# Kernel optimization log

Hardware: AMD Instinct MI355X
Metric: run time of the kernel (lower is better)

Reference implementation:

```python
import jax, jax.numpy as jnp
import numpy as np

N, E, B = 65536, 524288, 256
FEAT, EMB, NH, NB, NC = 64, 128, 4, 2, 4
OUT = EMB // NH
SLOPE = 0.01  # LeakyReLU negative_slope used everywhere in the module


def lrelu(x):
    return jnp.where(x > 0, x, SLOPE * x)


def seg_softmax(logits, seg, nseg, mask):
    # PyG softmax(src, batch): exp(x - segment_max) / (segment_sum + 1e-16)
    z = jnp.where(mask, logits, -jnp.inf)
    m = jax.ops.segment_max(z, seg, num_segments=nseg)
    m = jnp.where(jnp.isfinite(m), m, 0.0)
    e = jnp.exp(z - m[seg])
    s = jax.ops.segment_sum(e, seg, num_segments=nseg)
    return e / (s[seg] + 1e-16)


def topk_pool(x, seg, w, min_score, nseg):
    # PyG TopKPooling with min_score: score = softmax(x.w, batch);
    # keep nodes with score > min(min_score, per-graph max - 1e-7); x_out = x*score.
    score = x @ w  # [N]
    sm = seg_softmax(score, seg, nseg, jnp.ones(score.shape, bool))
    smax = jax.ops.segment_max(sm, seg, num_segments=nseg)
    thr = jnp.minimum(smax - 1e-7, min_score)
    keep = sm > thr[seg]
    xp = jnp.where(keep[:, None], x * sm[:, None], 0.0)
    return xp, keep


def graph_conv_max(x, src, dst, emask, Wrel, Wroot, b, n):
    # PyG GraphConv(aggr='max'): out = Wrel @ max_{j in N(i)} x_j + Wroot @ x_i + b
    msg = jnp.where(emask[:, None], x[src], -jnp.inf)  # [E, d]
    agg = jax.ops.segment_max(msg, dst, num_segments=n)
    agg = jnp.where(jnp.isfinite(agg), agg, 0.0)  # nodes with no in-edges -> 0 (PyG scatter fill)
    return agg @ Wrel.T + x @ Wroot.T + b


def batchnorm(x, g, b):
    # training-mode BatchNorm1d: batch statistics, biased variance, eps=1e-5
    mu = x.mean(0)
    var = x.var(0)
    return g * (x - mu) * jax.lax.rsqrt(var + 1e-5) + b


def setup_inputs() -> dict:
    key = jax.random.key(0)
    ks = jax.random.split(key, 16)
    s_feat = np.float32(1.0 / np.sqrt(FEAT))
    s_emb = np.float32(1.0 / np.sqrt(EMB))
    return {
        "x": jax.random.normal(ks[0], (N, FEAT), jnp.float32),
        "edge_index": jax.random.randint(ks[1], (2, E), 0, N, jnp.int32),
        "batch": (jnp.arange(N, dtype=jnp.int32) // (N // B)).astype(jnp.int32),
        "W_rel0": jax.random.normal(ks[2], (EMB, FEAT), jnp.float32) * s_feat,
        "W_root0": jax.random.normal(ks[3], (EMB, FEAT), jnp.float32) * s_feat,
        "b0": jnp.zeros((EMB,), jnp.float32),
        "bn0_g": jnp.ones((EMB,), jnp.float32),
        "bn0_b": jnp.zeros((EMB,), jnp.float32),
        "blk_pool_w": jax.random.normal(ks[4], (NB, NH, EMB), jnp.float32) * s_emb,
        "blk_Wrel": jax.random.normal(ks[5], (NB, NH, OUT, EMB), jnp.float32) * s_emb,
        "blk_Wroot": jax.random.normal(ks[6], (NB, NH, OUT, EMB), jnp.float32) * s_emb,
        "blk_b": jnp.zeros((NB, NH, OUT), jnp.float32),
        "blk_bn_g": jnp.ones((NB, EMB), jnp.float32),
        "blk_bn_b": jnp.zeros((NB, EMB), jnp.float32),
        "cls_pool_w": jax.random.normal(ks[7], (NC, EMB), jnp.float32) * s_emb,
        "cls_gW1": jax.random.normal(ks[8], (NC, EMB, EMB), jnp.float32) * s_emb,
        "cls_gb1": jnp.zeros((NC, EMB), jnp.float32),
        "cls_gW2": jax.random.normal(ks[9], (NC, EMB), jnp.float32) * s_emb,
        "cls_gb2": jnp.zeros((NC,), jnp.float32),
        "cls_fW1": jax.random.normal(ks[10], (NC, EMB, EMB), jnp.float32) * s_emb,
        "cls_fb1": jnp.zeros((NC, EMB), jnp.float32),
        "cls_fW2": jax.random.normal(ks[11], (NC, EMB), jnp.float32) * s_emb,
        "cls_fb2": jnp.zeros((NC,), jnp.float32),
        "batch_size": B,
    }


def reference(x, edge_index, batch, W_rel0, W_root0, b0, bn0_g, bn0_b,
              blk_pool_w, blk_Wrel, blk_Wroot, blk_b, blk_bn_g, blk_bn_b,
              cls_pool_w, cls_gW1, cls_gb1, cls_gW2, cls_gb2,
              cls_fW1, cls_fb1, cls_fW2, cls_fb2, batch_size):
    n = x.shape[0]
    src, dst = edge_index[0], edge_index[1]
    all_e = jnp.ones(src.shape, bool)
    # conv0 -> leaky_relu -> bn0
    h = lrelu(graph_conv_max(x, src, dst, all_e, W_rel0, W_root0, b0, n))
    cur = batchnorm(h, bn0_g, bn0_b)
    # multi-head blocks: pool (min_score=0.7) -> GraphConv(max) per head, scatter
    # back to original node slots, concat heads, bn, residual 0.5*(x + 0.5*bn(new))
    for bi in range(NB):
        heads = []
        for hi in range(NH):
            xp, keep = topk_pool(cur, batch, blk_pool_w[bi, hi], 0.7, batch_size)
            emask = keep[src] & keep[dst]
            o = lrelu(graph_conv_max(xp, src, dst, emask,
                                     blk_Wrel[bi, hi], blk_Wroot[bi, hi],
                                     blk_b[bi, hi], n))
            heads.append(jnp.where(keep[:, None], o, 0.0))
        new = batchnorm(jnp.concatenate(heads, axis=-1), blk_bn_g[bi], blk_bn_b[bi])
        cur = 0.5 * (cur + 0.5 * new)
    # classification heads: pool (min_score=0.8) -> GlobalAttention -> MLP -> 1
    outs = []
    for c in range(NC):
        xp, keep = topk_pool(cur, batch, cls_pool_w[c], 0.8, batch_size)
        gate = lrelu(xp @ cls_gW1[c].T + cls_gb1[c]) @ cls_gW2[c] + cls_gb2[c]  # [N]
        a = seg_softmax(gate, batch, batch_size, keep)
        pooled = jax.ops.segment_sum(a[:, None] * xp, batch, num_segments=batch_size)  # [B, EMB]
        y = lrelu(pooled @ cls_fW1[c].T + cls_fb1[c]) @ cls_fW2[c] + cls_fb2[c]  # [B]
        outs.append(y)
    logits = jnp.stack(outs, axis=-1)  # [B, NC]
    return jax.nn.log_softmax(logits, axis=-1)
```

## Files before the change

kernel.cpp:

```cpp
#include <hip/hip_runtime.h>
#include <math.h>

#define NN 65536
#define NE 524288
#define NG 256
#define SLOPE 0.01f
#define CAP 131072

__device__ __forceinline__ float lrelu(float v){ return v > 0.f ? v : SLOPE*v; }

__device__ __forceinline__ float blockMax4(float v, float* s4){
  #pragma unroll
  for(int o=32;o>0;o>>=1) v = fmaxf(v, __shfl_down(v, o, 64));
  int t = threadIdx.x;
  __syncthreads();
  if((t&63)==0) s4[t>>6] = v;
  __syncthreads();
  return fmaxf(fmaxf(s4[0], s4[1]), fmaxf(s4[2], s4[3]));
}
__device__ __forceinline__ float blockSum4(float v, float* s4){
  #pragma unroll
  for(int o=32;o>0;o>>=1) v += __shfl_down(v, o, 64);
  int t = threadIdx.x;
  __syncthreads();
  if((t&63)==0) s4[t>>6] = v;
  __syncthreads();
  return (s4[0]+s4[1])+(s4[2]+s4[3]);
}

__global__ __launch_bounds__(256) void k_count(const int* __restrict__ ei, int* __restrict__ deg){
  int e = blockIdx.x*256 + threadIdx.x;
  if(e < NE) atomicAdd(&deg[ei[NE + e]], 1);
}

__global__ __launch_bounds__(1024) void k_scan(const int* __restrict__ deg,
      int* __restrict__ offs, int* __restrict__ cursor){
  __shared__ int part[1024];
  int t = threadIdx.x;
  const int4* d4 = (const int4*)(deg + t*64);
  int4 buf[16];
  int s=0;
  #pragma unroll
  for(int i=0;i<16;i++){ buf[i]=d4[i]; s += buf[i].x+buf[i].y+buf[i].z+buf[i].w; }
  part[t]=s;
  __syncthreads();
  for(int off=1; off<1024; off<<=1){
    int v = (t>=off)? part[t-off] : 0;
    __syncthreads();
    part[t] += v;
    __syncthreads();
  }
  int run = (t==0)? 0 : part[t-1];
  #pragma unroll
  for(int i=0;i<16;i++){
    int4 d = buf[i];
    int4 o;
    o.x = run; run += d.x;
    o.y = run; run += d.y;
    o.z = run; run += d.z;
    o.w = run; run += d.w;
    ((int4*)(offs + t*64))[i] = o;
    ((int4*)(cursor + t*64))[i] = o;
  }
  if(t==1023) offs[NN] = run;
}

__global__ __launch_bounds__(256) void k_scatter(const int* __restrict__ ei,
      int* __restrict__ cursor, int* __restrict__ csr){
  int e = blockIdx.x*256 + threadIdx.x;
  if(e < NE){
    int d = ei[NE + e];
    int p = atomicAdd(&cursor[d], 1);
    csr[p] = ei[e];
  }
}

__global__ __launch_bounds__(256) void k_agg0(const float* __restrict__ x,
    const int* __restrict__ offs, const int* __restrict__ csr, float* __restrict__ agg0){
  int tid = blockIdx.x*256 + threadIdx.x;
  int node = tid>>4, q = tid&15;
  int e0 = offs[node], e1 = offs[node+1];
  float4 acc = make_float4(0.f,0.f,0.f,0.f);
  if(e0 < e1){
    acc = make_float4(-INFINITY,-INFINITY,-INFINITY,-INFINITY);
    int e = e0;
    for(; e+7 < e1; e += 8){
      int si[8];
      #pragma unroll
      for(int u=0;u<8;u++) si[u] = csr[e+u];
      float4 v[8];
      #pragma unroll
      for(int u=0;u<8;u++) v[u] = ((const float4*)x)[si[u]*16 + q];
      #pragma unroll
      for(int u=0;u<8;u++){
        acc.x=fmaxf(acc.x,v[u].x); acc.y=fmaxf(acc.y,v[u].y);
        acc.z=fmaxf(acc.z,v[u].z); acc.w=fmaxf(acc.w,v[u].w);
      }
    }
    for(; e < e1; e++){
      int s0 = csr[e];
      float4 v0 = ((const float4*)x)[s0*16 + q];
      acc.x=fmaxf(acc.x,v0.x); acc.y=fmaxf(acc.y,v0.y);
      acc.z=fmaxf(acc.z,v0.z); acc.w=fmaxf(acc.w,v0.w);
    }
  }
  ((float4*)agg0)[node*16 + q] = acc;
}

__global__ __launch_bounds__(256, 2) void k_conv0mm(
    const float* __restrict__ agg0, const float* __restrict__ x,
    const float* __restrict__ Wrel, const float* __restrict__ Wroot,
    const float* __restrict__ b0, float* __restrict__ cur,
    float* __restrict__ bnsum, float* __restrict__ bnsq){
  __shared__ float4 As[2048];
  const int t = threadIdx.x;
  const int tn = t & 15;
  const int tc = t >> 4;
  float acc[8][8];
  #pragma unroll
  for(int i=0;i<8;i++)
    #pragma unroll
    for(int j=0;j<8;j++) acc[i][j]=0.f;

  const size_t tileoff = (size_t)blockIdx.x * 8192;
  #pragma unroll 1
  for(int ch=0; ch<2; ch++){
    const float4* gA = (const float4*)((ch==0? agg0 : x) + tileoff);
    const float4* gW = (const float4*)(ch==0? Wrel : Wroot);
    __syncthreads();
    #pragma unroll
    for(int i=0;i<8;i++){
      int idx = t + i*256;
      int n = idx>>4, k4 = idx&15;
      As[n*16 + ((k4 + (n>>3))&15)] = gA[idx];
    }
    __syncthreads();
    #pragma unroll 1
    for(int k4=0;k4<16;k4++){
      float4 a4[8];
      #pragma unroll
      for(int i=0;i<8;i++) a4[i] = As[(tn*8+i)*16 + ((k4+tn)&15)];
      #pragma unroll
      for(int j=0;j<8;j++){
        float4 w4 = gW[(tc*8+j)*16 + k4];
        #pragma unroll
        for(int i=0;i<8;i++){
          acc[i][j] = fmaf(a4[i].x, w4.x, acc[i][j]);
          acc[i][j] = fmaf(a4[i].y, w4.y, acc[i][j]);
          acc[i][j] = fmaf(a4[i].z, w4.z, acc[i][j]);
          acc[i][j] = fmaf(a4[i].w, w4.w, acc[i][j]);
        }
      }
    }
  }

  float bj[8];
  #pragma unroll
  for(int j=0;j<8;j++) bj[j] = b0[tc*8+j];
  float cs[8], cq[8];
  #pragma unroll
  for(int j=0;j<8;j++){ cs[j]=0.f; cq[j]=0.f; }
  const int nbase = blockIdx.x*128;
  #pragma unroll
  for(int i=0;i<8;i++){
    int node = nbase + tn*8 + i;
    float v[8];
    #pragma unroll
    for(int j=0;j<8;j++){
      v[j] = lrelu(acc[i][j] + bj[j]);
      cs[j] += v[j]; cq[j] += v[j]*v[j];
    }
    float4 o0 = make_float4(v[0],v[1],v[2],v[3]);
    float4 o1 = make_float4(v[4],v[5],v[6],v[7]);
    ((float4*)cur)[node*32 + tc*2 + 0] = o0;
    ((float4*)cur)[node*32 + tc*2 + 1] = o1;
  }
  __syncthreads();
  float* reds = (float*)As;
  float* redq = ((float*)As) + 2048;
  #pragma unroll
  for(int j=0;j<8;j++){
    reds[(tc*8+j)*16 + tn] = cs[j];
    redq[(tc*8+j)*16 + tn] = cq[j];
  }
  __syncthreads();
  if(t<128){
    float S=0.f, Q=0.f;
    #pragma unroll
    for(int i=0;i<16;i++){ S += reds[t*16+i]; Q += redq[t*16+i]; }
    atomicAdd(&bnsum[t], S);
    atomicAdd(&bnsq[t], Q);
  }
}

__global__ __launch_bounds__(256) void k_scores(const float* __restrict__ cur0,
    const float* __restrict__ bns0, const float* __restrict__ bnq0,
    const float* __restrict__ g0,
    const float* __restrict__ pw0, const float* __restrict__ pw1,
    const float* __restrict__ pwc,
    float* __restrict__ scores0, float* __restrict__ pre1, float* __restrict__ pre2){
  __shared__ __align__(16) float w[12][128];
  __shared__ float sc0s[128];
  const int t = threadIdx.x;
  if(t<128){
    float mu = bns0[t]*(1.0f/NN);
    float var = bnq0[t]*(1.0f/NN) - mu*mu;
    sc0s[t] = g0[t]*rsqrtf(var+1e-5f);
  }
  __syncthreads();
  for(int i=t;i<512;i+=256){
    int h=i>>7, j=i&127;
    float s = sc0s[j];
    w[h][j]   = pw0[i]*s;
    w[4+h][j] = pw1[i]*(0.5f*s);
    w[8+h][j] = pwc[i]*(0.25f*s);
  }
  __syncthreads();
  const int tid = blockIdx.x*256 + t;
  const int n = tid>>5, k = tid&31;
  float4 v = ((const float4*)cur0)[tid];
  float a[12];
  #pragma unroll
  for(int q=0;q<12;q++){
    float4 wv = *(const float4*)&w[q][k*4];
    a[q] = v.x*wv.x + v.y*wv.y + v.z*wv.z + v.w*wv.w;
  }
  #pragma unroll
  for(int o=16;o>0;o>>=1){
    #pragma unroll
    for(int q=0;q<12;q++) a[q] += __shfl_down(a[q], o, 32);
  }
  if(k==0){
    ((float4*)scores0)[n] = make_float4(a[0],a[1],a[2],a[3]);
    ((float4*)pre1)[n]    = make_float4(a[4],a[5],a[6],a[7]);
    ((float4*)pre2)[n]    = make_float4(a[8],a[9],a[10],a[11]);
  }
}

__global__ __launch_bounds__(256) void k_poolselW(const float* __restrict__ scores,
    float minscore, float* __restrict__ sm4, int* __restrict__ cnt,
    int* __restrict__ wl, int* __restrict__ idxP){
  const int t = threadIdx.x, g = blockIdx.x;
  const int h = t>>6, l = t&63;
  const int n0 = g*256;
  float s[4];
  #pragma unroll
  for(int i=0;i<4;i++) s[i] = scores[(size_t)(n0 + l + i*64)*4 + h];
  float m = fmaxf(fmaxf(s[0],s[1]),fmaxf(s[2],s[3]));
  #pragma unroll
  for(int o=32;o>0;o>>=1) m = fmaxf(m, __shfl_xor(m, o, 64));
  float e[4], es=0.f;
  #pragma unroll
  for(int i=0;i<4;i++){ e[i]=expf(s[i]-m); es+=e[i]; }
  #pragma unroll
  for(int o=32;o>0;o>>=1) es += __shfl_xor(es, o, 64);
  float inv = 1.f/(es+1e-16f);
  float sm[4];
  float mx = -INFINITY;
  #pragma unroll
  for(int i=0;i<4;i++){ sm[i]=e[i]*inv; mx=fmaxf(mx,sm[i]); }
  #pragma unroll
  for(int o=32;o>0;o>>=1) mx = fmaxf(mx, __shfl_xor(mx, o, 64));
  float thr = fminf(mx - 1e-7f, minscore);
  #pragma unroll
  for(int i=0;i<4;i++){
    int n = n0 + l + i*64;
    sm4[(size_t)n*4 + h] = sm[i];
    int slot = -1;
    if(sm[i] > thr){
      int p = atomicAdd(cnt, 1);
      if(p < CAP){ slot = p; wl[p] = (h<<16) | n; }
    }
    idxP[(size_t)h*NN + n] = slot;
  }
}

__global__ __launch_bounds__(256) void k_blockconv0(const float* __restrict__ cur0,
    const int* __restrict__ offs, const int* __restrict__ csr,
    const int* __restrict__ idxP, const float* __restrict__ sm4,
    const int* __restrict__ cnt, const int* __restrict__ wl,
    const float* __restrict__ Wrel, const float* __restrict__ Wroot,
    const float* __restrict__ bias,
    float* __restrict__ new1c, float* __restrict__ bnsum, float* __restrict__ bnsq,
    const float* __restrict__ bns0, const float* __restrict__ bnq0,
    const float* __restrict__ g0, const float* __restrict__ b0bn){
  __shared__ __align__(16) float aggs[8][128];
  __shared__ __align__(16) float xps[8][128];
  __shared__ __align__(16) float scv[128];
  __shared__ __align__(16) float ofv[128];
  const int t = threadIdx.x, grp = t>>5, lane = t&31;
  if(t<128){
    float mu = bns0[t]*(1.0f/NN);
    float var = bnq0[t]*(1.0f/NN) - mu*mu;
    float sv = g0[t]*rsqrtf(var+1e-5f);
    scv[t]=sv; ofv[t]=b0bn[t]-mu*sv;
  }
  __syncthreads();
  const float4 s4l = *(const float4*)&scv[lane*4];
  const float4 o4l = *(const float4*)&ofv[lane*4];
  int total = *cnt; if(total > CAP) total = CAP;
  for(int item = blockIdx.x*8 + grp; item < total; item += gridDim.x*8){
    const int wv = wl[item];
    const int h = wv>>16, n = wv & 0xFFFF;
    const size_t hn = (size_t)h*NN;
    const float smn = sm4[(size_t)n*4+h];
    const int e0 = offs[n], e1 = offs[n+1];
    float4 acc = make_float4(-INFINITY,-INFINITY,-INFINITY,-INFINITY);
    bool any = false;
    for(int e=e0;e<e1;e++){
      int s = csr[e];
      if(idxP[hn + s] >= 0){
        any = true;
        float sv = sm4[(size_t)s*4+h];
        float4 v = ((const float4*)cur0)[s*32 + lane];
        v.x = (v.x*s4l.x + o4l.x)*sv; v.y = (v.y*s4l.y + o4l.y)*sv;
        v.z = (v.z*s4l.z + o4l.z)*sv; v.w = (v.w*s4l.w + o4l.w)*sv;
        acc.x = fmaxf(acc.x, v.x); acc.y = fmaxf(acc.y, v.y);
        acc.z = fmaxf(acc.z, v.z); acc.w = fmaxf(acc.w, v.w);
      }
    }
    if(!any) acc = make_float4(0.f,0.f,0.f,0.f);
    *(float4*)&aggs[grp][lane*4] = acc;
    float4 xv = ((const float4*)cur0)[n*32 + lane];
    xv.x = (xv.x*s4l.x + o4l.x)*smn; xv.y = (xv.y*s4l.y + o4l.y)*smn;
    xv.z = (xv.z*s4l.z + o4l.z)*smn; xv.w = (xv.w*s4l.w + o4l.w)*smn;
    *(float4*)&xps[grp][lane*4] = xv;
    const float* Wr = Wrel  + (size_t)(h*32+lane)*128;
    const float* Wo = Wroot + (size_t)(h*32+lane)*128;
    float o = bias[h*32+lane];
    for(int k=0;k<32;k++){
      float4 a  = *(const float4*)&aggs[grp][k*4];
      float4 xx = *(const float4*)&xps[grp][k*4];
      float4 wr = ((const float4*)Wr)[k];
      float4 wo = ((const float4*)Wo)[k];
      o += a.x*wr.x + a.y*wr.y + a.z*wr.z + a.w*wr.w;
      o += xx.x*wo.x + xx.y*wo.y + xx.z*wo.z + xx.w*wo.w;
    }
    o = lrelu(o);
    new1c[(size_t)item*32 + lane] = o;
    atomicAdd(&bnsum[h*32+lane], o);
    atomicAdd(&bnsq[h*32+lane], o*o);
  }
}

__global__ __launch_bounds__(256) void k_poolsel1(
    const float* __restrict__ pre1, float* __restrict__ pre2,
    const int* __restrict__ cnt0, const int* __restrict__ wl0,
    const float* __restrict__ new1c,
    const float* __restrict__ bnsA, const float* __restrict__ bnqA,
    const float* __restrict__ g1v,
    const float* __restrict__ pw1, const float* __restrict__ pwc,
    float minscore, float* __restrict__ sm4out,
    int* __restrict__ cnt1, int* __restrict__ wl1, int* __restrict__ idx1P){
  __shared__ float s1s[128];
  __shared__ __align__(16) float w1s[4][128];
  __shared__ __align__(16) float wcs[4][128];
  __shared__ float patch1[256][4];
  const int t = threadIdx.x, g = blockIdx.x;
  if(t<128){
    float mu = bnsA[t]*(1.0f/NN);
    float var = bnqA[t]*(1.0f/NN) - mu*mu;
    s1s[t] = g1v[t]*rsqrtf(var+1e-5f);
  }
  for(int i=t;i<512;i+=256){ w1s[i>>7][i&127]=pw1[i]; wcs[i>>7][i&127]=pwc[i]; }
  #pragma unroll
  for(int h=0;h<4;h++) patch1[t][h]=0.f;
  __syncthreads();
  int total0 = *cnt0; if(total0 > CAP) total0 = CAP;
  for(int i=t; i<total0; i+=256){
    int wv = wl0[i];
    int n = wv & 0xFFFF, hp = wv>>16;
    if((n>>8)==g){
      int nl = n & 255;
      float d[4]={0.f,0.f,0.f,0.f}, d2[4]={0.f,0.f,0.f,0.f};
      for(int l=0;l<32;l++){
        int j = hp*32+l;
        float base = new1c[(size_t)i*32+l] * s1s[j];
        #pragma unroll
        for(int h=0;h<4;h++){ d[h]+=base*w1s[h][j]; d2[h]+=base*wcs[h][j]; }
      }
      #pragma unroll
      for(int h=0;h<4;h++){
        atomicAdd(&patch1[nl][h], 0.25f*d[h]);
        atomicAdd(&pre2[n*4+h], 0.125f*d2[h]);
      }
    }
  }
  __syncthreads();
  const int h = t>>6, l = t&63;
  const int n0 = g*256;
  float s[4];
  #pragma unroll
  for(int i=0;i<4;i++){
    int nl = l + i*64;
    s[i] = pre1[(size_t)(n0+nl)*4 + h] + patch1[nl][h];
  }
  float m = fmaxf(fmaxf(s[0],s[1]),fmaxf(s[2],s[3]));
  #pragma unroll
  for(int o=32;o>0;o>>=1) m = fmaxf(m, __shfl_xor(m, o, 64));
  float e[4], es=0.f;
  #pragma unroll
  for(int i=0;i<4;i++){ e[i]=expf(s[i]-m); es+=e[i]; }
  #pragma unroll
  for(int o=32;o>0;o>>=1) es += __shfl_xor(es, o, 64);
  float inv = 1.f/(es+1e-16f);
  float sm[4];
  float mx = -INFINITY;
  #pragma unroll
  for(int i=0;i<4;i++){ sm[i]=e[i]*inv; mx=fmaxf(mx,sm[i]); }
  #pragma unroll
  for(int o=32;o>0;o>>=1) mx = fmaxf(mx, __shfl_xor(mx, o, 64));
  float thr = fminf(mx - 1e-7f, minscore);
  #pragma unroll
  for(int i=0;i<4;i++){
    int n = n0 + l + i*64;
    sm4out[(size_t)n*4 + h] = sm[i];
    int slot = -1;
    if(sm[i] > thr){
      int p = atomicAdd(cnt1, 1);
      if(p < CAP){ slot = p; wl1[p] = (h<<16) | n; }
    }
    idx1P[(size_t)h*NN + n] = slot;
  }
}

__global__ __launch_bounds__(256) void k_blockconv1(const float* __restrict__ cur0,
    const int* __restrict__ offs, const int* __restrict__ csr,
    const int* __restrict__ idx0P, const float* __restrict__ new1c,
    const int* __restrict__ idx1P, const float* __restrict__ sm41,
    const int* __restrict__ cnt1, const int* __restrict__ wl1,
    const float* __restrict__ Wrel, const float* __restrict__ Wroot,
    const float* __restrict__ bias,
    float* __restrict__ new2c, float* __restrict__ bnsum, float* __restrict__ bnsq,
    const float* __restrict__ bns0, const float* __restrict__ bnq0,
    const float* __restrict__ g0, const float* __restrict__ b0bn,
    const float* __restrict__ bnsA, const float* __restrict__ bnqA,
    const float* __restrict__ g1v, const float* __restrict__ b1v){
  __shared__ __align__(16) float aggs[8][128];
  __shared__ __align__(16) float xps[8][128];
  __shared__ __align__(16) float sc0s[128], of0s[128], s1s[128], o1s[128];
  const int t = threadIdx.x, grp = t>>5, lane = t&31;
  if(t<128){
    float mu = bns0[t]*(1.0f/NN);
    float var = bnq0[t]*(1.0f/NN) - mu*mu;
    float sv = g0[t]*rsqrtf(var+1e-5f);
    sc0s[t]=sv; of0s[t]=b0bn[t]-mu*sv;
    float mu1 = bnsA[t]*(1.0f/NN);
    float var1 = bnqA[t]*(1.0f/NN) - mu1*mu1;
    float s1 = g1v[t]*rsqrtf(var1+1e-5f);
    s1s[t]=s1; o1s[t]=b1v[t]-mu1*s1;
  }
  __syncthreads();
  const float4 s0l = *(const float4*)&sc0s[lane*4];
  const float4 o0l = *(const float4*)&of0s[lane*4];
  const float4 s1l = *(const float4*)&s1s[lane*4];
  const float4 o1l = *(const float4*)&o1s[lane*4];
  const int hb = lane>>3;
  const size_t hbn = (size_t)hb*NN;
  int total = *cnt1; if(total > CAP) total = CAP;
  for(int item = blockIdx.x*8 + grp; item < total; item += gridDim.x*8){
    const int wv = wl1[item];
    const int h = wv>>16, n = wv & 0xFFFF;
    const size_t hn = (size_t)h*NN;
    const float smn = sm41[(size_t)n*4+h];
    const int e0 = offs[n], e1 = offs[n+1];
    float4 acc = make_float4(-INFINITY,-INFINITY,-INFINITY,-INFINITY);
    bool any = false;
    for(int e=e0;e<e1;e++){
      int s = csr[e];
      if(idx1P[hn + s] >= 0){
        any = true;
        float sv = sm41[(size_t)s*4+h];
        float4 c0 = ((const float4*)cur0)[s*32 + lane];
        float4 v;
        v.x = 0.5f*(s0l.x*c0.x+o0l.x) + 0.25f*o1l.x;
        v.y = 0.5f*(s0l.y*c0.y+o0l.y) + 0.25f*o1l.y;
        v.z = 0.5f*(s0l.z*c0.z+o0l.z) + 0.25f*o1l.z;
        v.w = 0.5f*(s0l.w*c0.w+o0l.w) + 0.25f*o1l.w;
        int i0 = idx0P[hbn + s];
        if(i0 >= 0){
          float4 nv = ((const float4*)(new1c + (size_t)i0*32))[lane&7];
          v.x += 0.25f*s1l.x*nv.x; v.y += 0.25f*s1l.y*nv.y;
          v.z += 0.25f*s1l.z*nv.z; v.w += 0.25f*s1l.w*nv.w;
        }
        v.x*=sv; v.y*=sv; v.z*=sv; v.w*=sv;
        acc.x = fmaxf(acc.x, v.x); acc.y = fmaxf(acc.y, v.y);
        acc.z = fmaxf(acc.z, v.z); acc.w = fmaxf(acc.w, v.w);
      }
    }
    if(!any) acc = make_float4(0.f,0.f,0.f,0.f);
    *(float4*)&aggs[grp][lane*4] = acc;
    {
      float4 c0 = ((const float4*)cur0)[n*32 + lane];
      float4 v;
      v.x = 0.5f*(s0l.x*c0.x+o0l.x) + 0.25f*o1l.x;
      v.y = 0.5f*(s0l.y*c0.y+o0l.y) + 0.25f*o1l.y;
      v.z = 0.5f*(s0l.z*c0.z+o0l.z) + 0.25f*o1l.z;
      v.w = 0.5f*(s0l.w*c0.w+o0l.w) + 0.25f*o1l.w;
      int i0 = idx0P[hbn + n];
      if(i0 >= 0){
        float4 nv = ((const float4*)(new1c + (size_t)i0*32))[lane&7];
        v.x += 0.25f*s1l.x*nv.x; v.y += 0.25f*s1l.y*nv.y;
        v.z += 0.25f*s1l.z*nv.z; v.w += 0.25f*s1l.w*nv.w;
      }
      v.x*=smn; v.y*=smn; v.z*=smn; v.w*=smn;
      *(float4*)&xps[grp][lane*4] = v;
    }
    const float* Wr = Wrel  + (size_t)(h*32+lane)*128;
    const float* Wo = Wroot + (size_t)(h*32+lane)*128;
    float o = bias[h*32+lane];
    for(int k=0;k<32;k++){
      float4 a  = *(const float4*)&aggs[grp][k*4];
      float4 xx = *(const float4*)&xps[grp][k*4];
      float4 wr = ((const float4*)Wr)[k];
      float4 wo = ((const float4*)Wo)[k];
      o += a.x*wr.x + a.y*wr.y + a.z*wr.z + a.w*wr.w;
      o += xx.x*wo.x + xx.y*wo.y + xx.z*wo.z + xx.w*wo.w;
    }
    o = lrelu(o);
    new2c[(size_t)item*32 + lane] = o;
    atomicAdd(&bnsum[h*32+lane], o);
    atomicAdd(&bnsq[h*32+lane], o*o);
  }
}

__global__ __launch_bounds__(256) void k_cls2(const float* __restrict__ cur0,
    const int* __restrict__ idx0P, const float* __restrict__ new1c,
    const int* __restrict__ idx1P, const float* __restrict__ new2c,
    const float* __restrict__ pre2, const int* __restrict__ cnt1,
    const int* __restrict__ wl1, const float* __restrict__ pwc,
    const float* __restrict__ bns0, const float* __restrict__ bnq0,
    const float* __restrict__ g0, const float* __restrict__ b0bn,
    const float* __restrict__ bnsA, const float* __restrict__ bnqA,
    const float* __restrict__ g1v, const float* __restrict__ b1v,
    const float* __restrict__ bnsB, const float* __restrict__ bnqB,
    const float* __restrict__ g2v, const float* __restrict__ b2v,
    const float* __restrict__ gW1, const float* __restrict__ gb1,
    const float* __restrict__ gW2, const float* __restrict__ gb2,
    const float* __restrict__ fW1, const float* __restrict__ fb1,
    const float* __restrict__ fW2, const float* __restrict__ fb2,
    float* __restrict__ yws){
  __shared__ float red[4];
  __shared__ float sc0s[128], of0s[128], s1s[128], o1s[128], s2s[128], o2s[128];
  __shared__ float wc[128];
  __shared__ float patch[256];
  __shared__ int keptL[256];
  __shared__ float keptS[256];
  __shared__ float gateL[256];
  __shared__ __align__(16) float xk[128];
  __shared__ __align__(16) float pooled[128];
  __shared__ int nkept;
  const int t = threadIdx.x;
  const int g = blockIdx.x >> 2, c = blockIdx.x & 3;
  if(t<128){
    float mu = bns0[t]*(1.0f/NN);
    float var = bnq0[t]*(1.0f/NN) - mu*mu;
    float sv = g0[t]*rsqrtf(var+1e-5f);
    sc0s[t]=sv; of0s[t]=b0bn[t]-mu*sv;
    float mu1 = bnsA[t]*(1.0f/NN);
    float var1 = bnqA[t]*(1.0f/NN) - mu1*mu1;
    float s1 = g1v[t]*rsqrtf(var1+1e-5f);
    s1s[t]=s1; o1s[t]=b1v[t]-mu1*s1;
    float mu2 = bnsB[t]*(1.0f/NN);
    float var2 = bnqB[t]*(1.0f/NN) - mu2*mu2;
    float s2 = g2v[t]*rsqrtf(var2+1e-5f);
    s2s[t]=s2; o2s[t]=b2v[t]-mu2*s2;
    wc[t] = pwc[c*128+t];
  }
  patch[t]=0.f;
  __syncthreads();
  int total1 = *cnt1; if(total1 > CAP) total1 = CAP;
  for(int i=t; i<total1; i+=256){
    int wv = wl1[i];
    int n = wv & 0xFFFF, hp = wv>>16;
    if((n>>8)==g){
      float d=0.f;
      for(int l=0;l<32;l++){
        int j = hp*32+l;
        d += new2c[(size_t)i*32+l]*s2s[j]*wc[j];
      }
      atomicAdd(&patch[n&255], 0.25f*d);
    }
  }
  __syncthreads();
  const int n = g*256 + t;
  float sc = pre2[n*4 + c] + patch[t];
  float m = blockMax4(sc, red);
  float e = expf(sc-m);
  float ssum = blockSum4(e, red);
  float sm = e/(ssum+1e-16f);
  float smax = blockMax4(sm, red);
  float thr = fminf(smax - 1e-7f, 0.8f);
  if(t==0) nkept = 0;
  __syncthreads();
  if(sm > thr){
    int p = atomicAdd(&nkept,1);
    keptL[p]=t; keptS[p]=sm;
  }
  __syncthreads();
  const int K = nkept;
  for(int k=0;k<K;k++){
    int ln = keptL[k]; float sv = keptS[k];
    int nn = g*256 + ln;
    if(t<32){
      float4 c0 = ((const float4*)cur0)[nn*32 + t];
      float4 s0l = *(const float4*)&sc0s[t*4];
      float4 o0l = *(const float4*)&of0s[t*4];
      float4 s1l = *(const float4*)&s1s[t*4];
      float4 o1l = *(const float4*)&o1s[t*4];
      float4 s2l = *(const float4*)&s2s[t*4];
      float4 o2l = *(const float4*)&o2s[t*4];
      int hb = t>>3;
      float4 v1;
      v1.x = 0.5f*(s0l.x*c0.x+o0l.x) + 0.25f*o1l.x;
      v1.y = 0.5f*(s0l.y*c0.y+o0l.y) + 0.25f*o1l.y;
      v1.z = 0.5f*(s0l.z*c0.z+o0l.z) + 0.25f*o1l.z;
      v1.w = 0.5f*(s0l.w*c0.w+o0l.w) + 0.25f*o1l.w;
      int i0 = idx0P[(size_t)hb*NN + nn];
      if(i0 >= 0){
        float4 nv = ((const float4*)(new1c + (size_t)i0*32))[t&7];
        v1.x += 0.25f*s1l.x*nv.x; v1.y += 0.25f*s1l.y*nv.y;
        v1.z += 0.25f*s1l.z*nv.z; v1.w += 0.25f*s1l.w*nv.w;
      }
      float4 v2;
      v2.x = 0.5f*v1.x + 0.25f*o2l.x;
      v2.y = 0.5f*v1.y + 0.25f*o2l.y;
      v2.z = 0.5f*v1.z + 0.25f*o2l.z;
      v2.w = 0.5f*v1.w + 0.25f*o2l.w;
      int i1 = idx1P[(size_t)hb*NN + nn];
      if(i1 >= 0){
        float4 nv = ((const float4*)(new2c + (size_t)i1*32))[t&7];
        v2.x += 0.25f*s2l.x*nv.x; v2.y += 0.25f*s2l.y*nv.y;
        v2.z += 0.25f*s2l.z*nv.z; v2.w += 0.25f*s2l.w*nv.w;
      }
      v2.x*=sv; v2.y*=sv; v2.z*=sv; v2.w*=sv;
      *(float4*)&xk[t*4] = v2;
    }
    __syncthreads();
    float part = 0.f;
    if(t<128){
      const float* W = gW1 + (size_t)c*16384 + (size_t)t*128;
      float a = gb1[c*128+t];
      for(int f=0;f<32;f++){
        float4 xv = *(const float4*)&xk[f*4];
        float4 wv = ((const float4*)W)[f];
        a += xv.x*wv.x + xv.y*wv.y + xv.z*wv.z + xv.w*wv.w;
      }
      part = lrelu(a) * gW2[c*128+t];
    }
    float gs = blockSum4(part, red);
    if(t==0) gateL[k] = gs + gb2[c];
    __syncthreads();
  }
  float gv = (t<K)? gateL[t] : -INFINITY;
  float gm = blockMax4(gv, red);
  float ge = (t<K)? expf(gv-gm) : 0.f;
  float gsum = blockSum4(ge, red);
  if(t<K) gateL[t] = ge/(gsum+1e-16f);
  __syncthreads();
  if(t<128){
    int hb = t>>5, l = t&31;
    float acc = 0.f;
    for(int k=0;k<K;k++){
      int nn = g*256 + keptL[k];
      float c0 = cur0[(size_t)nn*128 + t];
      float v1 = 0.5f*(sc0s[t]*c0 + of0s[t]) + 0.25f*o1s[t];
      int i0 = idx0P[(size_t)hb*NN + nn];
      if(i0 >= 0) v1 += 0.25f*s1s[t]*new1c[(size_t)i0*32 + l];
      float v2 = 0.5f*v1 + 0.25f*o2s[t];
      int i1 = idx1P[(size_t)hb*NN + nn];
      if(i1 >= 0) v2 += 0.25f*s2s[t]*new2c[(size_t)i1*32 + l];
      acc += gateL[k]*keptS[k]*v2;
    }
    pooled[t]=acc;
  }
  __syncthreads();
  float part2=0.f;
  if(t<128){
    const float* F = fW1 + (size_t)c*16384 + (size_t)t*128;
    float a = fb1[c*128+t];
    for(int f=0;f<32;f++){
      float4 xv = *(const float4*)&pooled[f*4];
      float4 wv = ((const float4*)F)[f];
      a += xv.x*wv.x + xv.y*wv.y + xv.z*wv.z + xv.w*wv.w;
    }
    part2 = lrelu(a) * fW2[c*128+t];
  }
  float ysum = blockSum4(part2, red);
  if(t==0) yws[g*4+c] = ysum + fb2[c];
}

__global__ __launch_bounds__(256) void k_clsfin(const float* __restrict__ yws,
                                                float* __restrict__ out){
  const int g = threadIdx.x;
  float4 y = ((const float4*)yws)[g];
  float m = fmaxf(fmaxf(y.x,y.y), fmaxf(y.z,y.w));
  float l = logf(expf(y.x-m)+expf(y.y-m)+expf(y.z-m)+expf(y.w-m));
  ((float4*)out)[g] = make_float4(y.x-m-l, y.y-m-l, y.z-m-l, y.w-m-l);
}

extern "C" void kernel_launch(void* const* d_in, const int* in_sizes, int n_in,
                              void* d_out, int out_size, void* d_ws, size_t ws_size,
                              hipStream_t stream){
  (void)in_sizes; (void)n_in; (void)out_size; (void)ws_size;
  const float* x     = (const float*)d_in[0];
  const int*   ei    = (const int*)d_in[1];
  const float* Wrel0 = (const float*)d_in[3];
  const float* Wroot0= (const float*)d_in[4];
  const float* b0    = (const float*)d_in[5];
  const float* bn0g  = (const float*)d_in[6];
  const float* bn0b  = (const float*)d_in[7];
  const float* bpw   = (const float*)d_in[8];
  const float* bWrel = (const float*)d_in[9];
  const float* bWroot= (const float*)d_in[10];
  const float* bbv   = (const float*)d_in[11];
  const float* bbng  = (const float*)d_in[12];
  const float* bbnb  = (const float*)d_in[13];
  const float* cpw   = (const float*)d_in[14];
  const float* gW1   = (const float*)d_in[15];
  const float* gb1   = (const float*)d_in[16];
  const float* gW2   = (const float*)d_in[17];
  const float* gb2   = (const float*)d_in[18];
  const float* fW1   = (const float*)d_in[19];
  const float* fb1   = (const float*)d_in[20];
  const float* fW2   = (const float*)d_in[21];
  const float* fb2   = (const float*)d_in[22];

  char* ws = (char*)d_ws;
  float* cur0  = (float*)(ws + 0);
  float* new1c = (float*)(ws + 33554432ull);
  float* new2c = (float*)(ws + 50331648ull);
  float* agg0  = new2c;
  int*   csr   = (int*)(ws + 67108864ull);
  float* scores0=(float*)(ws + 69206016ull);
  float* sm40  = scores0;
  float* pre1  = (float*)(ws + 70254592ull);
  float* sm41  = pre1;
  float* pre2  = (float*)(ws + 71303168ull);
  int*   wl0   = (int*)(ws + 72351744ull);
  int*   wl1   = (int*)(ws + 72876032ull);
  int*   offs  = (int*)(ws + 73400320ull);
  int*   cursor= (int*)(ws + 73666560ull);
  int*   idx0P = (int*)(ws + 73928704ull);
  int*   idx1P = (int*)(ws + 74977280ull);
  char*  Z     = ws + 76025856ull;
  int*   deg   = (int*)Z;
  float* bnsum0= (float*)(Z + 262144);
  float* bnsq0 = (float*)(Z + 262656);
  float* bnA   = (float*)(Z + 263168);
  float* bqA   = (float*)(Z + 263680);
  float* bnB   = (float*)(Z + 264192);
  float* bqB   = (float*)(Z + 264704);
  int*   cnt0  = (int*)(Z + 265216);
  int*   cnt1  = (int*)(Z + 265220);
  float* yws   = (float*)(Z + 266240);

  hipMemsetAsync(Z, 0, 270336, stream);

  k_count  <<<2048,256,0,stream>>>(ei, deg);
  k_scan   <<<1,1024,0,stream>>>(deg, offs, cursor);
  k_scatter<<<2048,256,0,stream>>>(ei, cursor, csr);

  k_agg0    <<<4096,256,0,stream>>>(x, offs, csr, agg0);
  k_conv0mm <<<512,256,0,stream>>>(agg0, x, Wrel0, Wroot0, b0, cur0, bnsum0, bnsq0);

  k_scores<<<8192,256,0,stream>>>(cur0, bnsum0, bnsq0, bn0g,
                                  bpw, bpw + 512, cpw, scores0, pre1, pre2);

  k_poolselW<<<256,256,0,stream>>>(scores0, 0.7f, sm40, cnt0, wl0, idx0P);

  k_blockconv0<<<256,256,0,stream>>>(cur0, offs, csr, idx0P, sm40, cnt0, wl0,
                                     bWrel, bWroot, bbv, new1c, bnA, bqA,
                                     bnsum0, bnsq0, bn0g, bn0b);

  k_poolsel1<<<256,256,0,stream>>>(pre1, pre2, cnt0, wl0, new1c,
                                   bnA, bqA, bbng,
                                   bpw + 512, cpw,
                                   0.7f, sm41, cnt1, wl1, idx1P);

  k_blockconv1<<<256,256,0,stream>>>(cur0, offs, csr, idx0P, new1c,
                                     idx1P, sm41, cnt1, wl1,
                                     bWrel + 16384, bWroot + 16384, bbv + 128,
                                     new2c, bnB, bqB,
                                     bnsum0, bnsq0, bn0g, bn0b,
                                     bnA, bqA, bbng, bbnb);

  k_cls2<<<1024,256,0,stream>>>(cur0, idx0P, new1c, idx1P, new2c,
                                pre2, cnt1, wl1, cpw,
                                bnsum0, bnsq0, bn0g, bn0b,
                                bnA, bqA, bbng, bbnb,
                                bnB, bqB, bbng + 128, bbnb + 128,
                                gW1, gb1, gW2, gb2, fW1, fb1, fW2, fb2, yws);
  k_clsfin<<<1,256,0,stream>>>(yws, (float*)d_out);
}
```

Baseline: 379.5 us.

## Stage conv0 weights in LDS, pad agg0 gather tail, fuse final log-softmax

The layer-0 GEMM now stages the weight tile in shared memory with the same swizzle as the activations and partially unrolls the k loop, instead of reading weights from global memory in the inner loop. The CSR max-gather drops its scalar tail loop and clamps indices to the last edge, so every iteration does a full 8-wide batch. Repeated reads are harmless for a max. The final log-softmax kernel is removed: the last of the four class blocks per graph, detected with an atomic counter, computes it, which saves one launch. This doubles shared memory in the GEMM, which may reduce occupancy, and the tail now does some redundant loads.

```diff
diff --git a/kernel.cpp b/kernel.cpp
--- a/kernel.cpp
+++ b/kernel.cpp
@@ -83,11 +83,14 @@
   float4 acc = make_float4(0.f,0.f,0.f,0.f);
   if(e0 < e1){
     acc = make_float4(-INFINITY,-INFINITY,-INFINITY,-INFINITY);
-    int e = e0;
-    for(; e+7 < e1; e += 8){
+    const int last = e1 - 1;
+    for(int e=e0; e<e1; e+=8){
       int si[8];
       #pragma unroll
-      for(int u=0;u<8;u++) si[u] = csr[e+u];
+      for(int u=0;u<8;u++){
+        int ee = e+u; ee = ee<last? ee : last;
+        si[u] = csr[ee];
+      }
       float4 v[8];
       #pragma unroll
       for(int u=0;u<8;u++) v[u] = ((const float4*)x)[si[u]*16 + q];
@@ -97,12 +100,6 @@
         acc.z=fmaxf(acc.z,v[u].z); acc.w=fmaxf(acc.w,v[u].w);
       }
     }
-    for(; e < e1; e++){
-      int s0 = csr[e];
-      float4 v0 = ((const float4*)x)[s0*16 + q];
-      acc.x=fmaxf(acc.x,v0.x); acc.y=fmaxf(acc.y,v0.y);
-      acc.z=fmaxf(acc.z,v0.z); acc.w=fmaxf(acc.w,v0.w);
-    }
   }
   ((float4*)agg0)[node*16 + q] = acc;
 }
@@ -113,6 +110,7 @@
     const float* __restrict__ b0, float* __restrict__ cur,
     float* __restrict__ bnsum, float* __restrict__ bnsq){
   __shared__ float4 As[2048];
+  __shared__ float4 Ws[2048];
   const int t = threadIdx.x;
   const int tn = t & 15;
   const int tc = t >> 4;
@@ -132,25 +130,27 @@
     for(int i=0;i<8;i++){
       int idx = t + i*256;
       int n = idx>>4, k4 = idx&15;
-      As[n*16 + ((k4 + (n>>3))&15)] = gA[idx];
+      int sw = n*16 + ((k4 + (n>>3))&15);
+      As[sw] = gA[idx];
+      Ws[sw] = gW[idx];
     }
     __syncthreads();
-    #pragma unroll 1
+    #pragma unroll 4
     for(int k4=0;k4<16;k4++){
-      float4 a4[8];
+      float4 a4[8], w4[8];
       #pragma unroll
       for(int i=0;i<8;i++) a4[i] = As[(tn*8+i)*16 + ((k4+tn)&15)];
       #pragma unroll
-      for(int j=0;j<8;j++){
-        float4 w4 = gW[(tc*8+j)*16 + k4];
+      for(int i=0;i<8;i++) w4[i] = Ws[(tc*8+i)*16 + ((k4+tc)&15)];
+      #pragma unroll
+      for(int i=0;i<8;i++)
         #pragma unroll
-        for(int i=0;i<8;i++){
-          acc[i][j] = fmaf(a4[i].x, w4.x, acc[i][j]);
-          acc[i][j] = fmaf(a4[i].y, w4.y, acc[i][j]);
-          acc[i][j] = fmaf(a4[i].z, w4.z, acc[i][j]);
-          acc[i][j] = fmaf(a4[i].w, w4.w, acc[i][j]);
+        for(int j=0;j<8;j++){
+          acc[i][j] = fmaf(a4[i].x, w4[j].x, acc[i][j]);
+          acc[i][j] = fmaf(a4[i].y, w4[j].y, acc[i][j]);
+          acc[i][j] = fmaf(a4[i].z, w4[j].z, acc[i][j]);
+          acc[i][j] = fmaf(a4[i].w, w4[j].w, acc[i][j]);
         }
-      }
     }
   }
 
@@ -177,7 +177,7 @@
   }
   __syncthreads();
   float* reds = (float*)As;
-  float* redq = ((float*)As) + 2048;
+  float* redq = (float*)Ws;
   #pragma unroll
   for(int j=0;j<8;j++){
     reds[(tc*8+j)*16 + tn] = cs[j];
@@ -539,7 +539,7 @@
     const float* __restrict__ gW2, const float* __restrict__ gb2,
     const float* __restrict__ fW1, const float* __restrict__ fb1,
     const float* __restrict__ fW2, const float* __restrict__ fb2,
-    float* __restrict__ yws){
+    float* __restrict__ yws, int* __restrict__ gcnt, float* __restrict__ out){
   __shared__ float red[4];
   __shared__ float sc0s[128], of0s[128], s1s[128], o1s[128], s2s[128], o2s[128];
   __shared__ float wc[128];
@@ -687,16 +687,20 @@
     part2 = lrelu(a) * fW2[c*128+t];
   }
   float ysum = blockSum4(part2, red);
-  if(t==0) yws[g*4+c] = ysum + fb2[c];
-}
-
-__global__ __launch_bounds__(256) void k_clsfin(const float* __restrict__ yws,
-                                                float* __restrict__ out){
-  const int g = threadIdx.x;
-  float4 y = ((const float4*)yws)[g];
-  float m = fmaxf(fmaxf(y.x,y.y), fmaxf(y.z,y.w));
-  float l = logf(expf(y.x-m)+expf(y.y-m)+expf(y.z-m)+expf(y.w-m));
-  ((float4*)out)[g] = make_float4(y.x-m-l, y.y-m-l, y.z-m-l, y.w-m-l);
+  if(t==0){
+    yws[g*4+c] = ysum + fb2[c];
+    __threadfence();
+    int old = atomicAdd(&gcnt[g], 1);
+    if(old == 3){
+      __threadfence();
+      volatile float* yv = yws + g*4;
+      float y0=yv[0], y1=yv[1], y2=yv[2], y3=yv[3];
+      float mm = fmaxf(fmaxf(y0,y1), fmaxf(y2,y3));
+      float ll = logf(expf(y0-mm)+expf(y1-mm)+expf(y2-mm)+expf(y3-mm));
+      out[g*4+0]=y0-mm-ll; out[g*4+1]=y1-mm-ll;
+      out[g*4+2]=y2-mm-ll; out[g*4+3]=y3-mm-ll;
+    }
+  }
 }
 
 extern "C" void kernel_launch(void* const* d_in, const int* in_sizes, int n_in,
@@ -754,8 +758,9 @@
   int*   cnt0  = (int*)(Z + 265216);
   int*   cnt1  = (int*)(Z + 265220);
   float* yws   = (float*)(Z + 266240);
-
-  hipMemsetAsync(Z, 0, 270336, stream);
+  int*   gcnt  = (int*)(Z + 270336);
+
+  hipMemsetAsync(Z, 0, 271360, stream);
 
   k_count  <<<2048,256,0,stream>>>(ei, deg);
   k_scan   <<<1,1024,0,stream>>>(deg, offs, cursor);
@@ -790,6 +795,6 @@
                                 bnsum0, bnsq0, bn0g, bn0b,
                                 bnA, bqA, bbng, bbnb,
                                 bnB, bqB, bbng + 128, bbnb + 128,
-                                gW1, gb1, gW2, gb2, fW1, fb1, fW2, fb2, yws);
-  k_clsfin<<<1,256,0,stream>>>(yws, (float*)d_out);
-}
+                                gW1, gb1, gW2, gb2, fW1, fb1, fW2, fb2,
+                                yws, gcnt, (float*)d_out);
+}
```

New measurement: 386.0 us. Within noise of the previous version (+1.7%).
